# Optimization experiments

Hardware: AMD Instinct MI355X
Metric: run time of the kernel (lower is better)

The kernel has to match this reference:

```python
import jax, jax.numpy as jnp
import numpy as np

B, S, D, H = 2, 2048, 1024, 16
HD = D // H  # head_dim = 64


def setup_inputs() -> dict:
    key = jax.random.key(0)
    ks = jax.random.split(key, 12)
    w_scale = 1.0 / np.sqrt(D)
    return {
        "x": jax.random.normal(ks[0], (B, S, D), dtype=jnp.float32),
        "cause_mask": jax.random.randint(ks[1], (B, S), 0, 2) > 0,
        "effect_mask": jax.random.randint(ks[2], (B, S), 0, 2) > 0,
        "intervention_strength": jnp.float32(1.0),
        "Wq": jax.random.normal(ks[3], (D, D), dtype=jnp.float32) * w_scale,
        "bq": jnp.zeros((D,), dtype=jnp.float32),
        "Wk": jax.random.normal(ks[4], (D, D), dtype=jnp.float32) * w_scale,
        "bk": jnp.zeros((D,), dtype=jnp.float32),
        "Wv": jax.random.normal(ks[5], (D, D), dtype=jnp.float32) * w_scale,
        "bv": jnp.zeros((D,), dtype=jnp.float32),
        "Wo": jax.random.normal(ks[6], (D, D), dtype=jnp.float32) * w_scale,
        "bo": jnp.zeros((D,), dtype=jnp.float32),
    }


def reference(x, cause_mask, effect_mask, intervention_strength,
              Wq, bq, Wk, bk, Wv, bv, Wo, bo):
    b, s, d = x.shape
    # QKV projections -> [b, H, s, HD]
    q = (x @ Wq + bq).reshape(b, s, H, HD).transpose(0, 2, 1, 3)
    k = (x @ Wk + bk).reshape(b, s, H, HD).transpose(0, 2, 1, 3)
    v = (x @ Wv + bv).reshape(b, s, H, HD).transpose(0, 2, 1, 3)

    scores = jnp.einsum("bhqd,bhkd->bhqk", q, k) / jnp.sqrt(jnp.float32(HD))

    # Intervention mask: cause tokens on the query axis, effect on the key axis.
    # Faithful to source: both 'effect_to_cause' and 'cause_to_effect' are the
    # same boolean product, so multiplier = 1 - s*m + 0.5*s*m.
    cm = cause_mask[:, None, :, None]  # [b,1,s,1] query axis
    em = effect_mask[:, None, None, :]  # [b,1,1,s] key axis
    m = (cm & em).astype(scores.dtype)  # [b,1,s,s], broadcasts over heads
    imask = 1.0 - intervention_strength * m + 0.5 * intervention_strength * m
    scores = scores * imask

    attn = jax.nn.softmax(scores, axis=-1)  # dropout is identity in eval
    out = jnp.einsum("bhqk,bhkd->bhqd", attn, v)
    out = out.transpose(0, 2, 1, 3).reshape(b, s, d)
    return out @ Wo + bo
```

## Files before the change

kernel.cpp:

```cpp
#include <hip/hip_runtime.h>
#include <hip/hip_bf16.h>


typedef __attribute__((ext_vector_type(8))) short bf16x8;
typedef __attribute__((ext_vector_type(4))) float f32x4;

__device__ __forceinline__ unsigned short f2b(float f) {
  union { float f; unsigned u; } x; x.f = f;
  unsigned r = x.u + 0x7FFFu + ((x.u >> 16) & 1u);
  return (unsigned short)(r >> 16);
}

__device__ __forceinline__ unsigned short f2b_n(float f) {
  __hip_bfloat16 h = __float2bfloat16(f);
  union { __hip_bfloat16 h; unsigned short u; } c; c.h = h;
  return c.u;
}

__device__ __forceinline__ float fexp2(float x) {
#if __has_builtin(__builtin_amdgcn_exp2f)
  return __builtin_amdgcn_exp2f(x);
#else
  return __expf(x * 0.6931471805599453f);
#endif
}

__device__ __forceinline__ void gl_lds16(const unsigned short* g, unsigned short* l) {
  __builtin_amdgcn_global_load_lds(
      (const __attribute__((address_space(1))) unsigned int*)g,
      (__attribute__((address_space(3))) unsigned int*)l, 16, 0, 0);
}


__global__ __launch_bounds__(256) void cvt_x_kernel(const float* __restrict__ x,
                                                    unsigned short* __restrict__ xb, int n4) {
  int i = blockIdx.x * 256 + threadIdx.x;
  if (i >= n4) return;
  float4 v = ((const float4*)x)[i];
  ushort4 o;
  o.x = f2b(v.x); o.y = f2b(v.y); o.z = f2b(v.z); o.w = f2b(v.w);
  ((ushort4*)xb)[i] = o;
}

__global__ __launch_bounds__(256) void cvt_w4_kernel(
    const float* __restrict__ W0, const float* __restrict__ W1,
    const float* __restrict__ W2, const float* __restrict__ W3,
    unsigned short* __restrict__ WtBase) {
  __shared__ float t[64][33];
  const int z = blockIdx.z;
  const float* W = z == 0 ? W0 : (z == 1 ? W1 : (z == 2 ? W2 : W3));
  unsigned short* Wt = WtBase + (size_t)z * 1048576;
  const int k0 = blockIdx.x * 64, n0 = blockIdx.y * 32;
  const int tx = threadIdx.x, ty = threadIdx.y;
  #pragma unroll
  for (int i = 0; i < 8; i++)
    t[ty + i * 8][tx] = W[(size_t)(k0 + ty + i * 8) * 1024 + n0 + tx];
  __syncthreads();
  #pragma unroll
  for (int i = 0; i < 4; i++) {
    const int n = ty + i * 8;
    ushort2 pk;
    pk.x = f2b(t[tx * 2][n]);
    pk.y = f2b(t[tx * 2 + 1][n]);
    *(ushort2*)&Wt[(size_t)(n0 + n) * 1024 + k0 + tx * 2] = pk;
  }
}

template <int MODE>
__global__ __launch_bounds__(256) void gemm128(
    const unsigned short* __restrict__ A, const unsigned short* __restrict__ Bt,
    const float* __restrict__ b0, const float* __restrict__ b1, const float* __restrict__ b2,
    unsigned short* __restrict__ dq, unsigned short* __restrict__ dk,
    unsigned short* __restrict__ dv, float* __restrict__ dout) {
  __shared__ unsigned short As[2][4096];
  __shared__ unsigned short Bs[2][4096];
  const int tid = threadIdx.x;
  const int w = tid >> 6, lane = tid & 63;
  const int li = lane & 15, g = lane >> 4;
  const int wm = w >> 1, wn = w & 1;
  const int m0 = blockIdx.x * 128, n0 = blockIdx.y * 128;

  const int seg0 = w * 2, seg1 = w * 2 + 1;
  const int srow0 = seg0 * 16 + (lane >> 2), srow1 = seg1 * 16 + (lane >> 2);
  const int scol = (lane & 3) * 8;
  const unsigned short* gA0 = A + (size_t)(m0 + srow0) * 1024 + scol;
  const unsigned short* gA1 = A + (size_t)(m0 + srow1) * 1024 + scol;
  const unsigned short* gB0 = Bt + (size_t)(n0 + srow0) * 1024 + scol;
  const unsigned short* gB1 = Bt + (size_t)(n0 + srow1) * 1024 + scol;

  f32x4 acc[4][4];
  #pragma unroll
  for (int i = 0; i < 4; i++)
    #pragma unroll
    for (int j = 0; j < 4; j++) acc[i][j] = (f32x4){0.f, 0.f, 0.f, 0.f};

#define GSTAGE(bufi, kt)                                 \
  {                                                      \
    const int ko = (kt) * 32;                            \
    gl_lds16(gA0 + ko, &As[bufi][seg0 * 512]);           \
    gl_lds16(gA1 + ko, &As[bufi][seg1 * 512]);           \
    gl_lds16(gB0 + ko, &Bs[bufi][seg0 * 512]);           \
    gl_lds16(gB1 + ko, &Bs[bufi][seg1 * 512]);           \
  }

  GSTAGE(0, 0)
  int buf = 0;
  for (int kt = 0; kt < 32; kt++) {
    __syncthreads();
    if (kt + 1 < 32) GSTAGE(buf ^ 1, kt + 1)
    bf16x8 af[4], bfr[4];
    #pragma unroll
    for (int mt = 0; mt < 4; mt++)
      af[mt] = *(const bf16x8*)&As[buf][(wm * 64 + mt * 16 + li) * 32 + g * 8];
    #pragma unroll
    for (int nt = 0; nt < 4; nt++)
      bfr[nt] = *(const bf16x8*)&Bs[buf][(wn * 64 + nt * 16 + li) * 32 + g * 8];
    #pragma unroll
    for (int mt = 0; mt < 4; mt++)
      #pragma unroll
      for (int nt = 0; nt < 4; nt++)
        acc[mt][nt] = __builtin_amdgcn_mfma_f32_16x16x32_bf16(af[mt], bfr[nt], acc[mt][nt], 0, 0, 0);
    buf ^= 1;
  }
#undef GSTAGE

  if (MODE == 0) {
    const int sel = n0 >> 10;
    const float* bp = sel == 0 ? b0 : (sel == 1 ? b1 : b2);
    unsigned short* dst = sel == 0 ? dq : (sel == 1 ? dk : dv);
    #pragma unroll
    for (int nt = 0; nt < 4; nt++) {
      const int gc = n0 + wn * 64 + nt * 16 + li;
      const int c = gc & 1023, h = c >> 6, d = c & 63;
      const float bv = bp[c];
      #pragma unroll
      for (int mt = 0; mt < 4; mt++) {
        const int base = m0 + wm * 64 + mt * 16 + g * 4;
        const int bb = base >> 11, s = base & 2047;
        if (sel < 2) {
          #pragma unroll
          for (int r = 0; r < 4; r++)
            dst[((size_t)(bb * 16 + h) * 2048 + s + r) * 64 + d] = f2b_n(acc[mt][nt][r] + bv);
        } else {
          ushort4 pk;
          pk.x = f2b_n(acc[mt][nt][0] + bv);
          pk.y = f2b_n(acc[mt][nt][1] + bv);
          pk.z = f2b_n(acc[mt][nt][2] + bv);
          pk.w = f2b_n(acc[mt][nt][3] + bv);
          *(ushort4*)&dst[((size_t)(bb * 16 + h) * 64 + d) * 2048 + s] = pk;
        }
      }
    }
  } else {
    #pragma unroll
    for (int nt = 0; nt < 4; nt++) {
      const int gc = n0 + wn * 64 + nt * 16 + li;
      const float bv = b0[gc];
      #pragma unroll
      for (int mt = 0; mt < 4; mt++)
        #pragma unroll
        for (int r = 0; r < 4; r++) {
          const int gr = m0 + wm * 64 + mt * 16 + g * 4 + r;
          dout[(size_t)gr * 1024 + gc] = acc[mt][nt][r] + bv;
        }
    }
  }
}

__global__ __launch_bounds__(256, 4) void attn_kernel(
    const unsigned short* __restrict__ qb, const unsigned short* __restrict__ kb,
    const unsigned short* __restrict__ vtb, const int* __restrict__ cause,
    const int* __restrict__ effect, const float* __restrict__ strength,
    unsigned short* __restrict__ attb) {
  __shared__ unsigned short Ks[2][4096];
  __shared__ unsigned short Vs[2][4096];
  __shared__ unsigned short Pl[4][1024];
  const int tid = threadIdx.x;
  const int w = tid >> 6, lane = tid & 63;
  const int g = lane >> 4, li = lane & 15;
  const int lid = blockIdx.y * 32 + blockIdx.x;
  const int bh = ((lid & 7) << 2) | ((lid >> 3) & 3);
  const int qblk = lid >> 5;
  const int b = bh >> 4, h = bh & 15;
  const int q0 = qblk * 64 + w * 16;

  const unsigned short* kbp = kb + (size_t)bh * 2048 * 64;
  const unsigned short* vbp = vtb + (size_t)bh * 64 * 2048;

  const unsigned short* qrow = qb + ((size_t)bh * 2048 + q0 + li) * 64 + g * 8;
  const bf16x8 qa0 = *(const bf16x8*)(qrow);
  const bf16x8 qa1 = *(const bf16x8*)(qrow + 32);

  int cm[4];
  #pragma unroll
  for (int r = 0; r < 4; r++) cm[r] = cause[b * 2048 + q0 + g * 4 + r];
  const float LOG2E = 1.44269504f;
  const float fmask = 1.0f - 0.5f * strength[0];
  const float c0s2 = 0.125f * LOG2E;
  const float c1s2 = c0s2 * fmask;
  float mrr[4];
  #pragma unroll
  for (int r = 0; r < 4; r++) mrr[r] = cm[r] ? c1s2 : c0s2;
  const int* eff = effect + b * 2048;

  const int seg0 = w * 2, seg1 = w * 2 + 1;
  const int r0 = seg0 * 8 + (lane >> 3), r1 = seg1 * 8 + (lane >> 3);
  const int cs = (((lane & 7) ^ (lane >> 3)) * 8);
  const unsigned short* kg0 = kbp + (size_t)r0 * 64 + cs;
  const unsigned short* kg1 = kbp + (size_t)r1 * 64 + cs;
  const unsigned short* vg0 = vbp + (size_t)r0 * 2048 + cs;
  const unsigned short* vg1 = vbp + (size_t)r1 * 2048 + cs;

#define ASTAGE(bufi, t)                                        \
  {                                                            \
    gl_lds16(kg0 + (size_t)(t) * 4096, &Ks[bufi][seg0 * 512]); \
    gl_lds16(kg1 + (size_t)(t) * 4096, &Ks[bufi][seg1 * 512]); \
    gl_lds16(vg0 + (t) * 64, &Vs[bufi][seg0 * 512]);           \
    gl_lds16(vg1 + (t) * 64, &Vs[bufi][seg1 * 512]);           \
  }

  const int swz = (li & 7) << 4;
  const int col0 = ((g * 16) ^ swz) >> 1;
  const int col1 = ((64 + g * 16) ^ swz) >> 1;

  float l[4];
  f32x4 acc[4];
  #pragma unroll
  for (int r = 0; r < 4; r++) l[r] = 0.f;
  #pragma unroll
  for (int c = 0; c < 4; c++) acc[c] = (f32x4){0.f, 0.f, 0.f, 0.f};

  ASTAGE(0, 0)
  int buf = 0;
  for (int t = 0; t < 32; t++) {
    __syncthreads();
    if (t + 1 < 32) ASTAGE(buf ^ 1, t + 1)
    const int kk = t * 64;
    f32x4 s4[4];
    #pragma unroll
    for (int s = 0; s < 4; s++) {
      const bf16x8 kf0 = *(const bf16x8*)&Ks[buf][s * 1024 + li * 64 + col0];
      const bf16x8 kf1 = *(const bf16x8*)&Ks[buf][s * 1024 + li * 64 + col1];
      f32x4 z = (f32x4){0.f, 0.f, 0.f, 0.f};
      z = __builtin_amdgcn_mfma_f32_16x16x32_bf16(qa0, kf0, z, 0, 0, 0);
      z = __builtin_amdgcn_mfma_f32_16x16x32_bf16(qa1, kf1, z, 0, 0, 0);
      s4[s] = z;
    }
    float sv[4][4];
    #pragma unroll
    for (int s = 0; s < 4; s++) {
      const bool eb = eff[kk + s * 16 + li] != 0;
      #pragma unroll
      for (int r = 0; r < 4; r++) {
        sv[s][r] = fexp2(s4[s][r] * (eb ? mrr[r] : c0s2));
        l[r] += sv[s][r];
      }
    }
    #pragma unroll
    for (int s = 0; s < 4; s++)
      #pragma unroll
      for (int r = 0; r < 4; r++) {
        const int row = g * 4 + r;
        Pl[w][row * 64 + (((s * 32 + li * 2) ^ ((row & 7) << 4)) >> 1)] = f2b_n(sv[s][r]);
      }
    const bf16x8 pa0 = *(const bf16x8*)&Pl[w][li * 64 + col0];
    const bf16x8 pa1 = *(const bf16x8*)&Pl[w][li * 64 + col1];
    #pragma unroll
    for (int c = 0; c < 4; c++) {
      const bf16x8 vf0 = *(const bf16x8*)&Vs[buf][c * 1024 + li * 64 + col0];
      const bf16x8 vf1 = *(const bf16x8*)&Vs[buf][c * 1024 + li * 64 + col1];
      acc[c] = __builtin_amdgcn_mfma_f32_16x16x32_bf16(pa0, vf0, acc[c], 0, 0, 0);
      acc[c] = __builtin_amdgcn_mfma_f32_16x16x32_bf16(pa1, vf1, acc[c], 0, 0, 0);
    }
    buf ^= 1;
  }
#undef ASTAGE

  #pragma unroll
  for (int off = 1; off < 16; off <<= 1)
    #pragma unroll
    for (int r = 0; r < 4; r++) l[r] += __shfl_xor(l[r], off, 16);
  #pragma unroll
  for (int r = 0; r < 4; r++) l[r] = 1.0f / l[r];
  #pragma unroll
  for (int c = 0; c < 4; c++)
    #pragma unroll
    for (int r = 0; r < 4; r++) {
      const int row = q0 + g * 4 + r;
      attb[(size_t)(b * 2048 + row) * 1024 + h * 64 + c * 16 + li] = f2b_n(acc[c][r] * l[r]);
    }
}


extern "C" void kernel_launch(void* const* d_in, const int* in_sizes, int n_in,
                              void* d_out, int out_size, void* d_ws, size_t ws_size,
                              hipStream_t stream) {
  (void)in_sizes; (void)n_in; (void)out_size; (void)ws_size;
  const float* x = (const float*)d_in[0];
  const int* cause = (const int*)d_in[1];
  const int* effect = (const int*)d_in[2];
  const float* strength = (const float*)d_in[3];
  const float* Wq = (const float*)d_in[4];
  const float* bq = (const float*)d_in[5];
  const float* Wk = (const float*)d_in[6];
  const float* bk = (const float*)d_in[7];
  const float* Wv = (const float*)d_in[8];
  const float* bv = (const float*)d_in[9];
  const float* Wo = (const float*)d_in[10];
  const float* bo = (const float*)d_in[11];
  float* out = (float*)d_out;

  char* ws = (char*)d_ws;
  unsigned short* xb  = (unsigned short*)(ws);
  unsigned short* wqt = (unsigned short*)(ws + (8u << 20));
  unsigned short* qbf = (unsigned short*)(ws + (16u << 20));
  unsigned short* kbf = (unsigned short*)(ws + (24u << 20));
  unsigned short* vtb = (unsigned short*)(ws + (32u << 20));
  unsigned short* wot = wqt + 3u * 1048576u;
  unsigned short* attb = xb;

  cvt_x_kernel<<<4096, 256, 0, stream>>>(x, xb, 1048576);
  cvt_w4_kernel<<<dim3(16, 32, 4), dim3(32, 8), 0, stream>>>(Wq, Wk, Wv, Wo, wqt);

  gemm128<0><<<dim3(32, 24), 256, 0, stream>>>(xb, wqt, bq, bk, bv, qbf, kbf, vtb, nullptr);
  attn_kernel<<<dim3(32, 32), 256, 0, stream>>>(qbf, kbf, vtb, cause, effect, strength, attb);
  gemm128<1><<<dim3(32, 8), 256, 0, stream>>>(attb, wot, bo, nullptr, nullptr, nullptr, nullptr, nullptr, out);
}
```

Measured before the change: 225.5 us.

## Double per-wave query rows in attention and split output GEMM into smaller tiles

The attention kernel now gives each wave 32 query rows instead of 16, so every K/V tile loaded into LDS feeds twice the MFMA work, and the block count halves to 512. Launch bounds drop to 2 blocks per CU to leave room for the larger register and LDS footprint. The output projection moves to its own kernel with 128x64 tiles, doubling its grid to 512 blocks so the 256-CU device is better filled. The costs are lower attention occupancy and higher register pressure.

```diff
diff --git a/kernel.cpp b/kernel.cpp
--- a/kernel.cpp
+++ b/kernel.cpp
@@ -66,12 +66,11 @@
   }
 }
 
-template <int MODE>
-__global__ __launch_bounds__(256) void gemm128(
+__global__ __launch_bounds__(256) void gemm_qkv(
     const unsigned short* __restrict__ A, const unsigned short* __restrict__ Bt,
     const float* __restrict__ b0, const float* __restrict__ b1, const float* __restrict__ b2,
     unsigned short* __restrict__ dq, unsigned short* __restrict__ dk,
-    unsigned short* __restrict__ dv, float* __restrict__ dout) {
+    unsigned short* __restrict__ dv) {
   __shared__ unsigned short As[2][4096];
   __shared__ unsigned short Bs[2][4096];
   const int tid = threadIdx.x;
@@ -124,83 +123,138 @@
   }
 #undef GSTAGE
 
-  if (MODE == 0) {
-    const int sel = n0 >> 10;
-    const float* bp = sel == 0 ? b0 : (sel == 1 ? b1 : b2);
-    unsigned short* dst = sel == 0 ? dq : (sel == 1 ? dk : dv);
-    #pragma unroll
-    for (int nt = 0; nt < 4; nt++) {
-      const int gc = n0 + wn * 64 + nt * 16 + li;
-      const int c = gc & 1023, h = c >> 6, d = c & 63;
-      const float bv = bp[c];
-      #pragma unroll
-      for (int mt = 0; mt < 4; mt++) {
-        const int base = m0 + wm * 64 + mt * 16 + g * 4;
-        const int bb = base >> 11, s = base & 2047;
-        if (sel < 2) {
-          #pragma unroll
-          for (int r = 0; r < 4; r++)
-            dst[((size_t)(bb * 16 + h) * 2048 + s + r) * 64 + d] = f2b_n(acc[mt][nt][r] + bv);
-        } else {
-          ushort4 pk;
-          pk.x = f2b_n(acc[mt][nt][0] + bv);
-          pk.y = f2b_n(acc[mt][nt][1] + bv);
-          pk.z = f2b_n(acc[mt][nt][2] + bv);
-          pk.w = f2b_n(acc[mt][nt][3] + bv);
-          *(ushort4*)&dst[((size_t)(bb * 16 + h) * 64 + d) * 2048 + s] = pk;
-        }
+  const int sel = n0 >> 10;
+  const float* bp = sel == 0 ? b0 : (sel == 1 ? b1 : b2);
+  unsigned short* dst = sel == 0 ? dq : (sel == 1 ? dk : dv);
+  #pragma unroll
+  for (int nt = 0; nt < 4; nt++) {
+    const int gc = n0 + wn * 64 + nt * 16 + li;
+    const int c = gc & 1023, h = c >> 6, d = c & 63;
+    const float bv = bp[c];
+    #pragma unroll
+    for (int mt = 0; mt < 4; mt++) {
+      const int base = m0 + wm * 64 + mt * 16 + g * 4;
+      const int bb = base >> 11, s = base & 2047;
+      if (sel < 2) {
+        #pragma unroll
+        for (int r = 0; r < 4; r++)
+          dst[((size_t)(bb * 16 + h) * 2048 + s + r) * 64 + d] = f2b_n(acc[mt][nt][r] + bv);
+      } else {
+        ushort4 pk;
+        pk.x = f2b_n(acc[mt][nt][0] + bv);
+        pk.y = f2b_n(acc[mt][nt][1] + bv);
+        pk.z = f2b_n(acc[mt][nt][2] + bv);
+        pk.w = f2b_n(acc[mt][nt][3] + bv);
+        *(ushort4*)&dst[((size_t)(bb * 16 + h) * 64 + d) * 2048 + s] = pk;
       }
     }
-  } else {
-    #pragma unroll
-    for (int nt = 0; nt < 4; nt++) {
-      const int gc = n0 + wn * 64 + nt * 16 + li;
-      const float bv = b0[gc];
-      #pragma unroll
-      for (int mt = 0; mt < 4; mt++)
-        #pragma unroll
-        for (int r = 0; r < 4; r++) {
-          const int gr = m0 + wm * 64 + mt * 16 + g * 4 + r;
-          dout[(size_t)gr * 1024 + gc] = acc[mt][nt][r] + bv;
-        }
-    }
-  }
-}
-
-__global__ __launch_bounds__(256, 4) void attn_kernel(
+  }
+}
+
+__global__ __launch_bounds__(256) void gemm_out(
+    const unsigned short* __restrict__ A, const unsigned short* __restrict__ Bt,
+    const float* __restrict__ bias, float* __restrict__ dout) {
+  __shared__ unsigned short As[2][4096];
+  __shared__ unsigned short Bs[2][2048];
+  const int tid = threadIdx.x;
+  const int w = tid >> 6, lane = tid & 63;
+  const int li = lane & 15, g = lane >> 4;
+  const int m0 = blockIdx.x * 128, n0 = blockIdx.y * 64;
+
+  const int srow0 = w * 32 + (lane >> 2), srow1 = w * 32 + 16 + (lane >> 2);
+  const int srowB = w * 16 + (lane >> 2);
+  const int scol = (lane & 3) * 8;
+  const unsigned short* gA0 = A + (size_t)(m0 + srow0) * 1024 + scol;
+  const unsigned short* gA1 = A + (size_t)(m0 + srow1) * 1024 + scol;
+  const unsigned short* gB0 = Bt + (size_t)(n0 + srowB) * 1024 + scol;
+
+  f32x4 acc[2][4];
+  #pragma unroll
+  for (int i = 0; i < 2; i++)
+    #pragma unroll
+    for (int j = 0; j < 4; j++) acc[i][j] = (f32x4){0.f, 0.f, 0.f, 0.f};
+
+#define OSTAGE(bufi, kt)                                 \
+  {                                                      \
+    const int ko = (kt) * 32;                            \
+    gl_lds16(gA0 + ko, &As[bufi][w * 1024]);             \
+    gl_lds16(gA1 + ko, &As[bufi][w * 1024 + 512]);       \
+    gl_lds16(gB0 + ko, &Bs[bufi][w * 512]);              \
+  }
+
+  OSTAGE(0, 0)
+  int buf = 0;
+  for (int kt = 0; kt < 32; kt++) {
+    __syncthreads();
+    if (kt + 1 < 32) OSTAGE(buf ^ 1, kt + 1)
+    bf16x8 af[2], bfr[4];
+    #pragma unroll
+    for (int mt = 0; mt < 2; mt++)
+      af[mt] = *(const bf16x8*)&As[buf][(w * 32 + mt * 16 + li) * 32 + g * 8];
+    #pragma unroll
+    for (int nt = 0; nt < 4; nt++)
+      bfr[nt] = *(const bf16x8*)&Bs[buf][(nt * 16 + li) * 32 + g * 8];
+    #pragma unroll
+    for (int mt = 0; mt < 2; mt++)
+      #pragma unroll
+      for (int nt = 0; nt < 4; nt++)
+        acc[mt][nt] = __builtin_amdgcn_mfma_f32_16x16x32_bf16(af[mt], bfr[nt], acc[mt][nt], 0, 0, 0);
+    buf ^= 1;
+  }
+#undef OSTAGE
+
+  #pragma unroll
+  for (int nt = 0; nt < 4; nt++) {
+    const int gc = n0 + nt * 16 + li;
+    const float bv = bias[gc];
+    #pragma unroll
+    for (int mt = 0; mt < 2; mt++)
+      #pragma unroll
+      for (int r = 0; r < 4; r++) {
+        const int gr = m0 + w * 32 + mt * 16 + g * 4 + r;
+        dout[(size_t)gr * 1024 + gc] = acc[mt][nt][r] + bv;
+      }
+  }
+}
+
+__global__ __launch_bounds__(256, 2) void attn_kernel(
     const unsigned short* __restrict__ qb, const unsigned short* __restrict__ kb,
     const unsigned short* __restrict__ vtb, const int* __restrict__ cause,
     const int* __restrict__ effect, const float* __restrict__ strength,
     unsigned short* __restrict__ attb) {
   __shared__ unsigned short Ks[2][4096];
   __shared__ unsigned short Vs[2][4096];
-  __shared__ unsigned short Pl[4][1024];
+  __shared__ unsigned short Pl[4][2048];
   const int tid = threadIdx.x;
   const int w = tid >> 6, lane = tid & 63;
   const int g = lane >> 4, li = lane & 15;
-  const int lid = blockIdx.y * 32 + blockIdx.x;
+  const int lid = blockIdx.y * 16 + blockIdx.x;
   const int bh = ((lid & 7) << 2) | ((lid >> 3) & 3);
   const int qblk = lid >> 5;
   const int b = bh >> 4, h = bh & 15;
-  const int q0 = qblk * 64 + w * 16;
+  const int q0 = qblk * 128 + w * 32;
 
   const unsigned short* kbp = kb + (size_t)bh * 2048 * 64;
   const unsigned short* vbp = vtb + (size_t)bh * 64 * 2048;
 
-  const unsigned short* qrow = qb + ((size_t)bh * 2048 + q0 + li) * 64 + g * 8;
-  const bf16x8 qa0 = *(const bf16x8*)(qrow);
-  const bf16x8 qa1 = *(const bf16x8*)(qrow + 32);
-
-  int cm[4];
-  #pragma unroll
-  for (int r = 0; r < 4; r++) cm[r] = cause[b * 2048 + q0 + g * 4 + r];
+  bf16x8 qa[2][2];
+  #pragma unroll
+  for (int i = 0; i < 2; i++) {
+    const unsigned short* qrow = qb + ((size_t)bh * 2048 + q0 + i * 16 + li) * 64 + g * 8;
+    qa[i][0] = *(const bf16x8*)(qrow);
+    qa[i][1] = *(const bf16x8*)(qrow + 32);
+  }
+
   const float LOG2E = 1.44269504f;
   const float fmask = 1.0f - 0.5f * strength[0];
   const float c0s2 = 0.125f * LOG2E;
   const float c1s2 = c0s2 * fmask;
-  float mrr[4];
-  #pragma unroll
-  for (int r = 0; r < 4; r++) mrr[r] = cm[r] ? c1s2 : c0s2;
+  float mrr[2][4];
+  #pragma unroll
+  for (int i = 0; i < 2; i++)
+    #pragma unroll
+    for (int r = 0; r < 4; r++)
+      mrr[i][r] = cause[b * 2048 + q0 + i * 16 + g * 4 + r] ? c1s2 : c0s2;
   const int* eff = effect + b * 2048;
 
   const int seg0 = w * 2, seg1 = w * 2 + 1;
@@ -223,12 +277,15 @@
   const int col0 = ((g * 16) ^ swz) >> 1;
   const int col1 = ((64 + g * 16) ^ swz) >> 1;
 
-  float l[4];
-  f32x4 acc[4];
-  #pragma unroll
-  for (int r = 0; r < 4; r++) l[r] = 0.f;
-  #pragma unroll
-  for (int c = 0; c < 4; c++) acc[c] = (f32x4){0.f, 0.f, 0.f, 0.f};
+  float l[2][4];
+  f32x4 acc[2][4];
+  #pragma unroll
+  for (int i = 0; i < 2; i++) {
+    #pragma unroll
+    for (int r = 0; r < 4; r++) l[i][r] = 0.f;
+    #pragma unroll
+    for (int c = 0; c < 4; c++) acc[i][c] = (f32x4){0.f, 0.f, 0.f, 0.f};
+  }
 
   ASTAGE(0, 0)
   int buf = 0;
@@ -236,41 +293,40 @@
     __syncthreads();
     if (t + 1 < 32) ASTAGE(buf ^ 1, t + 1)
     const int kk = t * 64;
-    f32x4 s4[4];
     #pragma unroll
     for (int s = 0; s < 4; s++) {
       const bf16x8 kf0 = *(const bf16x8*)&Ks[buf][s * 1024 + li * 64 + col0];
       const bf16x8 kf1 = *(const bf16x8*)&Ks[buf][s * 1024 + li * 64 + col1];
-      f32x4 z = (f32x4){0.f, 0.f, 0.f, 0.f};
-      z = __builtin_amdgcn_mfma_f32_16x16x32_bf16(qa0, kf0, z, 0, 0, 0);
-      z = __builtin_amdgcn_mfma_f32_16x16x32_bf16(qa1, kf1, z, 0, 0, 0);
-      s4[s] = z;
+      const bool eb = eff[kk + s * 16 + li] != 0;
+      #pragma unroll
+      for (int i = 0; i < 2; i++) {
+        f32x4 z = (f32x4){0.f, 0.f, 0.f, 0.f};
+        z = __builtin_amdgcn_mfma_f32_16x16x32_bf16(qa[i][0], kf0, z, 0, 0, 0);
+        z = __builtin_amdgcn_mfma_f32_16x16x32_bf16(qa[i][1], kf1, z, 0, 0, 0);
+        #pragma unroll
+        for (int r = 0; r < 4; r++) {
+          const float p = fexp2(z[r] * (eb ? mrr[i][r] : c0s2));
+          l[i][r] += p;
+          const int row = i * 16 + g * 4 + r;
+          Pl[w][row * 64 + (((s * 32 + li * 2) ^ ((row & 7) << 4)) >> 1)] = f2b_n(p);
+        }
+      }
     }
-    float sv[4][4];
-    #pragma unroll
-    for (int s = 0; s < 4; s++) {
-      const bool eb = eff[kk + s * 16 + li] != 0;
-      #pragma unroll
-      for (int r = 0; r < 4; r++) {
-        sv[s][r] = fexp2(s4[s][r] * (eb ? mrr[r] : c0s2));
-        l[r] += sv[s][r];
-      }
+    bf16x8 pa[2][2];
+    #pragma unroll
+    for (int i = 0; i < 2; i++) {
+      pa[i][0] = *(const bf16x8*)&Pl[w][(i * 16 + li) * 64 + col0];
+      pa[i][1] = *(const bf16x8*)&Pl[w][(i * 16 + li) * 64 + col1];
     }
-    #pragma unroll
-    for (int s = 0; s < 4; s++)
-      #pragma unroll
-      for (int r = 0; r < 4; r++) {
-        const int row = g * 4 + r;
-        Pl[w][row * 64 + (((s * 32 + li * 2) ^ ((row & 7) << 4)) >> 1)] = f2b_n(sv[s][r]);
-      }
-    const bf16x8 pa0 = *(const bf16x8*)&Pl[w][li * 64 + col0];
-    const bf16x8 pa1 = *(const bf16x8*)&Pl[w][li * 64 + col1];
     #pragma unroll
     for (int c = 0; c < 4; c++) {
       const bf16x8 vf0 = *(const bf16x8*)&Vs[buf][c * 1024 + li * 64 + col0];
       const bf16x8 vf1 = *(const bf16x8*)&Vs[buf][c * 1024 + li * 64 + col1];
-      acc[c] = __builtin_amdgcn_mfma_f32_16x16x32_bf16(pa0, vf0, acc[c], 0, 0, 0);
-      acc[c] = __builtin_amdgcn_mfma_f32_16x16x32_bf16(pa1, vf1, acc[c], 0, 0, 0);
+      #pragma unroll
+      for (int i = 0; i < 2; i++) {
+        acc[i][c] = __builtin_amdgcn_mfma_f32_16x16x32_bf16(pa[i][0], vf0, acc[i][c], 0, 0, 0);
+        acc[i][c] = __builtin_amdgcn_mfma_f32_16x16x32_bf16(pa[i][1], vf1, acc[i][c], 0, 0, 0);
+      }
     }
     buf ^= 1;
   }
@@ -279,16 +335,22 @@
   #pragma unroll
   for (int off = 1; off < 16; off <<= 1)
     #pragma unroll
-    for (int r = 0; r < 4; r++) l[r] += __shfl_xor(l[r], off, 16);
-  #pragma unroll
-  for (int r = 0; r < 4; r++) l[r] = 1.0f / l[r];
-  #pragma unroll
-  for (int c = 0; c < 4; c++)
-    #pragma unroll
-    for (int r = 0; r < 4; r++) {
-      const int row = q0 + g * 4 + r;
-      attb[(size_t)(b * 2048 + row) * 1024 + h * 64 + c * 16 + li] = f2b_n(acc[c][r] * l[r]);
-    }
+    for (int i = 0; i < 2; i++)
+      #pragma unroll
+      for (int r = 0; r < 4; r++) l[i][r] += __shfl_xor(l[i][r], off, 16);
+  #pragma unroll
+  for (int i = 0; i < 2; i++)
+    #pragma unroll
+    for (int r = 0; r < 4; r++) l[i][r] = 1.0f / l[i][r];
+  #pragma unroll
+  for (int i = 0; i < 2; i++)
+    #pragma unroll
+    for (int c = 0; c < 4; c++)
+      #pragma unroll
+      for (int r = 0; r < 4; r++) {
+        const int row = q0 + i * 16 + g * 4 + r;
+        attb[(size_t)(b * 2048 + row) * 1024 + h * 64 + c * 16 + li] = f2b_n(acc[i][c][r] * l[i][r]);
+      }
 }
 
 
@@ -322,7 +384,7 @@
   cvt_x_kernel<<<4096, 256, 0, stream>>>(x, xb, 1048576);
   cvt_w4_kernel<<<dim3(16, 32, 4), dim3(32, 8), 0, stream>>>(Wq, Wk, Wv, Wo, wqt);
 
-  gemm128<0><<<dim3(32, 24), 256, 0, stream>>>(xb, wqt, bq, bk, bv, qbf, kbf, vtb, nullptr);
-  attn_kernel<<<dim3(32, 32), 256, 0, stream>>>(qbf, kbf, vtb, cause, effect, strength, attb);
-  gemm128<1><<<dim3(32, 8), 256, 0, stream>>>(attb, wot, bo, nullptr, nullptr, nullptr, nullptr, nullptr, out);
-}
+  gemm_qkv<<<dim3(32, 24), 256, 0, stream>>>(xb, wqt, bq, bk, bv, qbf, kbf, vtb);
+  attn_kernel<<<dim3(16, 32), 256, 0, stream>>>(qbf, kbf, vtb, cause, effect, strength, attb);
+  gemm_out<<<dim3(32, 16), 256, 0, stream>>>(attb, wot, bo, out);
+}
```

New measurement: 219.6 us. -2.6%, faster.
